# Optimization experiments

Measured on AMD Instinct MI355X. Metric: run time of the kernel, lower is better.

Reference implementation:

```python
import jax, jax.numpy as jnp
import numpy as np

D_IN, D, BOX, REL, THR = 2048, 512, 8, 80, 0.5

def _ln(x, g, b):
    m = jnp.mean(x, -1, keepdims=True)
    v = jnp.mean((x - m) ** 2, -1, keepdims=True)
    return (x - m) * jax.lax.rsqrt(v + 1e-5) * g + b

def setup_inputs():
    key = jax.random.key(0)
    ks = jax.random.split(key, 24)
    B, N = 32, 50
    def lin(k, i, o):
        return jax.random.normal(k, (i, o), jnp.float32) / np.sqrt(i)
    z = lambda n: jnp.zeros((n,), jnp.float32)
    o = lambda n: jnp.ones((n,), jnp.float32)
    return {
        "images": jax.random.normal(ks[0], (B, N, D_IN), jnp.float32),
        "selfbbox": jax.random.uniform(ks[1], (B, N, BOX), jnp.float32),
        "bbox": jax.random.uniform(ks[2], (B, N, N, BOX), jnp.float32),
        "pre_w": lin(ks[3], D_IN, D), "pre_b": z(D), "pre_g": o(D), "pre_be": z(D),
        "subj_w": lin(ks[4], D, D), "subj_b": z(D),
        "obj_w": lin(ks[5], D, D), "obj_b": z(D),
        "ps1_w": lin(ks[6], BOX, 64), "ps1_b": z(64), "ps_g": o(64), "ps_be": z(64),
        "ps2_w": lin(ks[7], 64, 64), "ps2_b": z(64),
        "pr1_w": lin(ks[8], BOX, 64), "pr1_b": z(64), "pr_g": o(64), "pr_be": z(64),
        "pr2_w": lin(ks[9], 64, 64), "pr2_b": z(64),
        "rs_w": lin(ks[10], D + 64, 1), "rs_b": z(1),
        "rf_w": lin(ks[11], D + 64, REL), "rf_b": z(REL),
        "g1_w": lin(ks[12], D + REL, D + REL), "g1_b": z(D + REL),
        "g2_w": lin(ks[13], D + REL, D), "g2_b": z(D),
        "g3_w": lin(ks[14], D, D), "g3_b": z(D),
    }

def reference(images, selfbbox, bbox, pre_w, pre_b, pre_g, pre_be, subj_w, subj_b,
              obj_w, obj_b, ps1_w, ps1_b, ps_g, ps_be, ps2_w, ps2_b,
              pr1_w, pr1_b, pr_g, pr_be, pr2_w, pr2_b, rs_w, rs_b, rf_w, rf_b,
              g1_w, g1_b, g2_w, g2_b, g3_w, g3_b):
    B, N = images.shape[0], images.shape[1]
    mask = jnp.sum(images, -1) != 0.0                      # [B,N] valid nodes
    attention_mask = (~mask)[:, None, None, :]             # [B,1,1,N]
    mf = mask.astype(images.dtype)
    # preprocess: Linear -> ReLU -> (dropout=id at eval) -> LayerNorm
    x = _ln(jax.nn.relu(images @ pre_w + pre_b), pre_g, pre_be)  # [B,N,512]
    x_subj = jax.nn.relu(x @ subj_w + subj_b) * mf[..., None]
    x_obj = jax.nn.relu(x @ obj_w + obj_b) * mf[..., None]
    eye = jnp.eye(N, dtype=bool)
    # pairwise subject/object features: diag(i==j) holds subject, off-diag object j
    x_rela = jnp.where(eye[None, :, :, None], x_subj[:, :, None, :], x_obj[:, None, :, :])
    x_rela = x_rela * mf[:, :, None, None]
    # positional MLPs
    h = jax.nn.relu(selfbbox @ ps1_w + ps1_b)
    h = jax.nn.relu(_ln(h, ps_g, ps_be) @ ps2_w + ps2_b)
    pos_self = h * mf[..., None]
    h = jax.nn.relu(bbox @ pr1_w + pr1_b)
    h = jax.nn.relu(_ln(h, pr_g, pr_be) @ pr2_w + pr2_b)
    pos_relas = h * mf[:, None, :, None] * mf[:, :, None, None]
    pos_rela = jnp.where(eye[None, :, :, None], pos_self[:, :, None, :], pos_relas)
    pos_rela = pos_rela * mf[:, :, None, None]
    pair = jnp.concatenate([x_rela, pos_rela], axis=-1)    # [B,N,N,576]
    pair_mask = mask[:, :, None] & mask[:, None, :]        # [B,N,N]
    # Relationshipness: pairwise relatedness score p + attention-pooled relation feats
    logits = (pair @ rs_w + rs_b)[..., 0]                  # [B,N,N]
    p = jax.nn.sigmoid(logits) * pair_mask.astype(images.dtype)
    attn = jax.nn.softmax(jnp.where(pair_mask, logits, -1e9), axis=2)
    feat = jax.nn.relu(pair @ rf_w + rf_b)                 # [B,N,N,80]
    relas = jnp.einsum('bij,bijf->bif', attn, feat) * mf[..., None]
    xx = jnp.concatenate([x, relas], axis=-1)              # [B,N,592]
    # dynamic edge threshold -> block-diagonal graph, expressed densely per image
    A = p > THR                                            # edge i->j
    Ahat = A | eye[None]                                   # add remaining self loops
    Af = Ahat.astype(xx.dtype)
    deg = jnp.sum(Af, axis=1)                              # in-degree at target j (>=1)
    dinv = jax.lax.rsqrt(deg)
    An = Af * dinv[:, :, None] * dinv[:, None, :]          # sym-normalized adjacency
    def gcn(hh, w, b):
        return jnp.einsum('bij,bif->bjf', An, hh @ w) + b
    x1 = jax.nn.relu(gcn(xx, g1_w, g1_b))
    x2 = jax.nn.relu(gcn(x1, g2_w, g2_b))
    x3 = jax.nn.relu(gcn(x2, g3_w, g3_b))
    outs = jnp.concatenate([x[:, None], x3[:, None]], axis=1)  # [B,2,N,512]
    return (outs, attention_mask)
```

## Files before the change

### kernel.cpp

```cpp
#include <hip/hip_runtime.h>
#include <hip/hip_bf16.h>

typedef __hip_bfloat16 bf16;

#define BB 32
#define NN 50
#define DIN 2048
#define DD 512
#define PD 64
#define FF 80
#define GG 592
#define BN (BB*NN)

#define O_FLAG  0
#define O_MF    16
#define O_SS    1616
#define O_SO    3216
#define O_PS    4816
#define O_FS    107216
#define O_FO    235216
#define O_RL    363216
#define O_LG    491216
#define O_AN    571216
#define O_T     651216
#define O_X1    1598416
#define O_X2    2545616
#define O_WPRE  3364816
#define O_BPRE  4413392
#define O_GPRE  4413904
#define O_EPRE  4414416
#define O_WSUBJ 4414928
#define O_BSUBJ 4677072
#define O_WOBJ  4677584
#define O_BOBJ  4939728
#define O_WPS1  4940240
#define O_BPS1  4940752
#define O_GPS   4940816
#define O_EPS   4940880
#define O_WPS2  4940944
#define O_BPS2  4945040
#define O_WPR1  4945104
#define O_BPR1  4945616
#define O_GPR   4945680
#define O_EPR   4945744
#define O_WPR2  4945808
#define O_BPR2  4949904
#define O_WRS   4949968
#define O_BRS   4950544
#define O_WRF   4950560
#define O_BRF   4996640
#define O_WG1   4996736
#define O_BG1   5347200
#define O_WG2   5347792
#define O_BG2   5650896
#define O_WG3   5651408
#define O_BG3   5913552
#define O_FT    5914064

#define PSLICE  819200

__device__ __forceinline__ float b2f(bf16 x){ return __bfloat162float(x); }

__device__ __forceinline__ float LDI(const bf16* p, size_t i, int f32m){
    if(f32m){
        bf16 a=p[2*i], b=p[2*i+1];
        unsigned short lo,hi;
        __builtin_memcpy(&lo,&a,2); __builtin_memcpy(&hi,&b,2);
        unsigned v=((unsigned)hi<<16)|(unsigned)lo;
        float f; __builtin_memcpy(&f,&v,4);
        return f;
    }
    return __bfloat162float(p[i]);
}

__global__ void k_flag(const bf16* __restrict__ images, float* __restrict__ ws){
    __shared__ int cnt;
    if(threadIdx.x==0) cnt=0;
    __syncthreads();
    bf16 h=images[2*threadIdx.x];
    unsigned short u; __builtin_memcpy(&u,&h,2);
    unsigned e=(u>>7)&0xFF;
    int sane=((u&0x7FFF)==0 || (e>=0x70&&e<=0x85))?1:0;
    atomicAdd(&cnt,sane);
    __syncthreads();
    if(threadIdx.x==0) ws[O_FLAG]=(cnt<48)?1.f:0.f;
}

__device__ __forceinline__ void conv(const bf16* s, float* d, int n, int F, int i0, int st){
    for(int g=i0; g<n; g+=st) d[g]=LDI(s,(size_t)g,F);
}
__global__ void kw(const bf16* p0,const bf16* p1,const bf16* p2,const bf16* p3,
                   const bf16* p4,const bf16* p5,const bf16* p6,const bf16* p7,
                   const bf16* p8,const bf16* p9,const bf16* p10,const bf16* p11,
                   const bf16* p12,const bf16* p13,const bf16* p14,const bf16* p15,
                   const bf16* p16,const bf16* p17,const bf16* p18,const bf16* p19,
                   const bf16* p20,const bf16* p21,const bf16* p22,const bf16* p23,
                   const bf16* p24,const bf16* p25,const bf16* p26,const bf16* p27,
                   const bf16* p28,const bf16* p29, float* __restrict__ ws){
    int F=ws[O_FLAG]>0.5f;
    int i0=blockIdx.x*256+threadIdx.x, st=gridDim.x*256;
    conv(p0, ws+O_WPRE, 1048576,F,i0,st);
    conv(p1, ws+O_BPRE, 512,F,i0,st);
    conv(p2, ws+O_GPRE, 512,F,i0,st);
    conv(p3, ws+O_EPRE, 512,F,i0,st);
    conv(p4, ws+O_WSUBJ,262144,F,i0,st);
    conv(p5, ws+O_BSUBJ,512,F,i0,st);
    conv(p6, ws+O_WOBJ, 262144,F,i0,st);
    conv(p7, ws+O_BOBJ, 512,F,i0,st);
    conv(p8, ws+O_WPS1, 512,F,i0,st);
    conv(p9, ws+O_BPS1, 64,F,i0,st);
    conv(p10,ws+O_GPS,  64,F,i0,st);
    conv(p11,ws+O_EPS,  64,F,i0,st);
    conv(p12,ws+O_WPS2, 4096,F,i0,st);
    conv(p13,ws+O_BPS2, 64,F,i0,st);
    conv(p14,ws+O_WPR1, 512,F,i0,st);
    conv(p15,ws+O_BPR1, 64,F,i0,st);
    conv(p16,ws+O_GPR,  64,F,i0,st);
    conv(p17,ws+O_EPR,  64,F,i0,st);
    conv(p18,ws+O_WPR2, 4096,F,i0,st);
    conv(p19,ws+O_BPR2, 64,F,i0,st);
    conv(p20,ws+O_WRS,  576,F,i0,st);
    conv(p21,ws+O_BRS,  1,F,i0,st);
    conv(p22,ws+O_WRF,  46080,F,i0,st);
    conv(p23,ws+O_BRF,  80,F,i0,st);
    conv(p24,ws+O_WG1,  350464,F,i0,st);
    conv(p25,ws+O_BG1,  592,F,i0,st);
    conv(p26,ws+O_WG2,  303104,F,i0,st);
    conv(p27,ws+O_BG2,  512,F,i0,st);
    conv(p28,ws+O_WG3,  262144,F,i0,st);
    conv(p29,ws+O_BG3,  512,F,i0,st);
}

__global__ void __launch_bounds__(256,4) k_x(const bf16* __restrict__ images,
                                             float* __restrict__ ws){
    __shared__ float as[8*256];
    __shared__ float rsum[4][8];
    int blk=blockIdx.x, t=threadIdx.x;
    int rg=blk>>3, ks=blk&7;
    int r0=rg*8, kbase=ks*256;
    int F=ws[O_FLAG]>0.5f;
    int wv=t>>6, ln=t&63;
    float sv[8];
    #pragma unroll
    for(int row=0;row<8;row++){
        float v=LDI(images,(size_t)(r0+row)*DIN+kbase+t,F);
        as[row*256+t]=v;
        sv[row]=v;
    }
    #pragma unroll
    for(int row=0;row<8;row++){
        float s=sv[row];
        for(int m=32;m>0;m>>=1) s+=__shfl_xor(s,m,64);
        sv[row]=s;
    }
    if(ln==0){
        #pragma unroll
        for(int row=0;row<8;row++) rsum[wv][row]=sv[row];
    }
    __syncthreads();
    if(t<8){
        float s=rsum[0][t]+rsum[1][t]+rsum[2][t]+rsum[3][t];
        ws[O_RL+(size_t)(r0+t)*8+ks]=s;
    }
    const float* wP=ws+O_WPRE+(size_t)kbase*DD;
    int c0=t, c1=t+256;
    float acc[8][2]={};
    for(int k0=0;k0<256;k0+=8){
        float w0[8],w1[8];
        #pragma unroll
        for(int u=0;u<8;u++){ w0[u]=wP[(size_t)(k0+u)*DD+c0]; w1[u]=wP[(size_t)(k0+u)*DD+c1]; }
        #pragma unroll
        for(int row=0;row<8;row++){
            float4 a0=*(const float4*)&as[row*256+k0];
            float4 a1=*(const float4*)&as[row*256+k0+4];
            acc[row][0]+=a0.x*w0[0]; acc[row][1]+=a0.x*w1[0];
            acc[row][0]+=a0.y*w0[1]; acc[row][1]+=a0.y*w1[1];
            acc[row][0]+=a0.z*w0[2]; acc[row][1]+=a0.z*w1[2];
            acc[row][0]+=a0.w*w0[3]; acc[row][1]+=a0.w*w1[3];
            acc[row][0]+=a1.x*w0[4]; acc[row][1]+=a1.x*w1[4];
            acc[row][0]+=a1.y*w0[5]; acc[row][1]+=a1.y*w1[5];
            acc[row][0]+=a1.z*w0[6]; acc[row][1]+=a1.z*w1[6];
            acc[row][0]+=a1.w*w0[7]; acc[row][1]+=a1.w*w1[7];
        }
    }
    float* P=ws + ((ks<7)? (O_FT+(size_t)ks*PSLICE) : (size_t)O_T);
    #pragma unroll
    for(int row=0;row<8;row++){
        size_t b=(size_t)(r0+row)*DD;
        P[b+c0]=acc[row][0]; P[b+c1]=acc[row][1];
    }
}

__global__ void __launch_bounds__(256,4) k_xr(float* __restrict__ ws, float* __restrict__ out){
    __shared__ float red[256];
    int blk=blockIdx.x, t=threadIdx.x;
    int r0=blk*4;
    if(t<4){
        int r=r0+t;
        float s=0.f;
        for(int ks=0;ks<8;ks++) s+=ws[O_RL+(size_t)r*8+ks];
        float mf=(s!=0.f)?1.f:0.f;
        ws[O_MF+r]=mf;
        out[(size_t)BB*2*NN*DD+r]=1.f-mf;
    }
    const float* bPre=ws+O_BPRE; const float* gPre=ws+O_GPRE; const float* ePre=ws+O_EPRE;
    int c0=t, c1=t+256;
    for(int row=0;row<4;row++){
        int r=r0+row;
        float y0=bPre[c0], y1=bPre[c1];
        for(int ks=0;ks<8;ks++){
            const float* P=ws + ((ks<7)? (O_FT+(size_t)ks*PSLICE) : (size_t)O_T);
            y0+=P[(size_t)r*DD+c0]; y1+=P[(size_t)r*DD+c1];
        }
        y0=fmaxf(y0,0.f); y1=fmaxf(y1,0.f);
        red[t]=y0+y1; __syncthreads();
        for(int o=128;o>0;o>>=1){ if(t<o) red[t]+=red[t+o]; __syncthreads(); }
        float mean=red[0]/DD; __syncthreads();
        float d0=y0-mean, d1=y1-mean;
        red[t]=d0*d0+d1*d1; __syncthreads();
        for(int o=128;o>0;o>>=1){ if(t<o) red[t]+=red[t+o]; __syncthreads(); }
        float rstd=rsqrtf(red[0]/DD+1e-5f);
        __syncthreads();
        float xv0=d0*rstd*gPre[c0]+ePre[c0];
        float xv1=d1*rstd*gPre[c1]+ePre[c1];
        size_t ob=((size_t)(r/NN)*2)*NN*DD+(size_t)(r%NN)*DD;
        out[ob+c0]=xv0; out[ob+c1]=xv1;
    }
}

__global__ void __launch_bounds__(256,4) k_so1(const float* __restrict__ out,
                                               float* __restrict__ ws){
    __shared__ float xs[4*DD];
    __shared__ float mrow_s[4];
    int blk=blockIdx.x, t=threadIdx.x;
    int rg=blk>>2, mat=(blk>>1)&1, ch=blk&1;
    int r0=rg*4;
    for(int idx=t; idx<4*DD; idx+=256){
        int row=idx>>9, k=idx&511;
        int r=r0+row;
        xs[idx]=out[((size_t)(r/NN)*2)*NN*DD+(size_t)(r%NN)*DD+k];
    }
    if(t<4) mrow_s[t]=ws[O_MF+r0+t];
    __syncthreads();
    const float* W =ws+(mat?O_WOBJ:O_WSUBJ);
    const float* Bb=ws+(mat?O_BOBJ:O_BSUBJ);
    int c=ch*256+t;
    float acc[4]={0.f,0.f,0.f,0.f};
    for(int k0=0;k0<DD;k0+=8){
        float w[8];
        #pragma unroll
        for(int u=0;u<8;u++) w[u]=W[(size_t)(k0+u)*DD+c];
        #pragma unroll
        for(int row=0;row<4;row++){
            float4 a0=*(const float4*)&xs[row*DD+k0];
            float4 a1=*(const float4*)&xs[row*DD+k0+4];
            acc[row]+=a0.x*w[0]; acc[row]+=a0.y*w[1];
            acc[row]+=a0.z*w[2]; acc[row]+=a0.w*w[3];
            acc[row]+=a1.x*w[4]; acc[row]+=a1.y*w[5];
            acc[row]+=a1.z*w[6]; acc[row]+=a1.w*w[7];
        }
    }
    float* Y=ws+O_FT+(size_t)mat*PSLICE;
    #pragma unroll
    for(int row=0;row<4;row++)
        Y[(size_t)(r0+row)*DD+c]=fmaxf(acc[row]+Bb[c],0.f)*mrow_s[row];
}

__global__ void __launch_bounds__(256,4) k_so2(float* __restrict__ ws){
    __shared__ float yl[4][DD];
    int blk=blockIdx.x, t=threadIdx.x, wv=t>>6, ln=t&63;
    int combo=blk*4+wv;
    int mat=combo&1, r=combo>>1;
    const float* Y=ws+O_FT+(size_t)mat*PSLICE+(size_t)r*DD;
    for(int k=ln;k<DD;k+=64) yl[wv][k]=Y[k];
    __syncthreads();
    const float* wRs=ws+O_WRS;
    float ps=0.f;
    for(int k=ln;k<DD;k+=64) ps+=yl[wv][k]*wRs[k];
    for(int m=32;m>0;m>>=1) ps+=__shfl_xor(ps,m,64);
    if(ln==0) ws[(mat?O_SO:O_SS)+r]=ps;
    const float* wRf=ws+O_WRF;
    float* dst=ws+(mat?O_FO:O_FS)+(size_t)r*FF;
    {
        float a=0.f;
        for(int k0=0;k0<DD;k0+=4){
            float4 y4=*(const float4*)&yl[wv][k0];
            a+=y4.x*wRf[(size_t)k0*FF+ln];
            a+=y4.y*wRf[(size_t)(k0+1)*FF+ln];
            a+=y4.z*wRf[(size_t)(k0+2)*FF+ln];
            a+=y4.w*wRf[(size_t)(k0+3)*FF+ln];
        }
        dst[ln]=a;
    }
    if(ln<16){
        int c=64+ln;
        float a=0.f;
        for(int k0=0;k0<DD;k0+=4){
            float4 y4=*(const float4*)&yl[wv][k0];
            a+=y4.x*wRf[(size_t)k0*FF+c];
            a+=y4.y*wRf[(size_t)(k0+1)*FF+c];
            a+=y4.z*wRf[(size_t)(k0+2)*FF+c];
            a+=y4.w*wRf[(size_t)(k0+3)*FF+c];
        }
        dst[c]=a;
    }
}

__global__ void k_pos_self(const bf16* __restrict__ sb, float* __restrict__ ws){
    __shared__ float h[PD];
    __shared__ float stat[2];
    int r=blockIdx.x, t=threadIdx.x;
    int F=ws[O_FLAG]>0.5f;
    const float* w1=ws+O_WPS1;
    float acc=0.f;
    for(int q=0;q<8;q++) acc+=LDI(sb,(size_t)r*8+q,F)*w1[q*PD+t];
    acc=fmaxf(acc+ws[O_BPS1+t],0.f);
    h[t]=acc; __syncthreads();
    if(t==0){
        float sm=0; for(int k=0;k<PD;k++) sm+=h[k];
        float mean=sm/PD;
        float v=0; for(int k=0;k<PD;k++){float d=h[k]-mean; v+=d*d;}
        stat[0]=mean; stat[1]=rsqrtf(v/PD+1e-5f);
    }
    __syncthreads();
    float hn=(acc-stat[0])*stat[1]*ws[O_GPS+t]+ws[O_EPS+t];
    h[t]=hn; __syncthreads();
    float a2=0.f;
    const float* w2=ws+O_WPS2;
    for(int k=0;k<PD;k++) a2+=h[k]*w2[k*PD+t];
    ws[O_PS+(size_t)r*PD+t]=fmaxf(a2+ws[O_BPS2+t],0.f)*ws[O_MF+r];
}

#define PSTRIDE 68
#define ZROW(m) ((m)*PSTRIDE + (((m)>>3)<<2))

__global__ void __launch_bounds__(256,3) k_pair(const bf16* __restrict__ bbox,
                                                float* __restrict__ ws){
    __shared__ float zp[64*PSTRIDE+64];
    __shared__ float wbuf[80*PSTRIDE];
    __shared__ float w1s[512];
    __shared__ float bbs[512];
    __shared__ float b1s[64], g1s[64], be1s[64], b2s[64], wrss[64];
    __shared__ float brfs[80];
    __shared__ float rowmi[64], rowmj[64], rowbase[64];
    __shared__ int   rowfb[64], rowps[64], rowdg[64];

    int t=threadIdx.x;
    int blk=blockIdx.x;
    int F=ws[O_FLAG]>0.5f;
    float rsb=ws[O_BRS];

    float wrfreg[20];
    #pragma unroll
    for(int u=0;u<20;u++){
        int idx=t+256*u;
        int f=idx>>6, k=idx&63;
        wrfreg[u]=ws[O_WRF+(size_t)(512+k)*FF+f];
    }

    for(int idx=t; idx<4096; idx+=256){ int k=idx>>6, c=idx&63; wbuf[k*PSTRIDE+c]=ws[O_WPR2+idx]; }
    for(int idx=t; idx<512; idx+=256) w1s[idx]=ws[O_WPR1+idx];
    for(int idx=t; idx<512; idx+=256) bbs[idx]=LDI(bbox,(size_t)blk*512+idx,F);
    if(t<64){
        b1s[t]=ws[O_BPR1+t]; g1s[t]=ws[O_GPR+t]; be1s[t]=ws[O_EPR+t];
        b2s[t]=ws[O_BPR2+t]; wrss[t]=ws[O_WRS+512+t];
    } else if(t<144){
        brfs[t-64]=ws[O_BRF+t-64];
    }
    if(t<64){
        int p=blk*64+t;
        int r=p/NN, j=p-r*NN;
        int b=r/NN, i=r-b*NN;
        int dg=(i==j);
        rowmi[t]=ws[O_MF+r];
        rowmj[t]=ws[O_MF+b*NN+j];
        rowdg[t]=dg;
        rowbase[t]=dg? ws[O_SS+r] : ws[O_SO+b*NN+j];
        rowfb[t]=dg? (O_FS+r*FF) : (O_FO+(b*NN+j)*FF);
        rowps[t]=O_PS+r*PD;
    }
    __syncthreads();

    int wv=t>>6, ln=t&63;
    #pragma unroll 2
    for(int q=0;q<16;q++){
        int m=wv*16+q;
        float acc=0.f;
        #pragma unroll
        for(int u=0;u<8;u++) acc+=bbs[m*8+u]*w1s[u*64+ln];
        float h1=fmaxf(acc+b1s[ln],0.f);
        float sm=h1;
        for(int o=32;o>0;o>>=1) sm+=__shfl_xor(sm,o,64);
        float mean=sm*(1.f/64.f);
        float d=h1-mean;
        float vv=d*d;
        for(int o=32;o>0;o>>=1) vv+=__shfl_xor(vv,o,64);
        float rstd=rsqrtf(vv*(1.f/64.f)+1e-5f);
        zp[ZROW(m)+ln]=d*rstd*g1s[ln]+be1s[ln];
    }

    int tr=t>>4, tc=t&15;
    int m0=tr*4, c0=tc*4;
    float a1[4][4]={};
    #pragma unroll 2
    for(int k0=0;k0<64;k0+=4){
        float4 zv[4], wvv[4];
        #pragma unroll
        for(int i=0;i<4;i++) zv[i]=*(const float4*)&zp[ZROW(m0+i)+k0];
        #pragma unroll
        for(int u=0;u<4;u++) wvv[u]=*(const float4*)&wbuf[(k0+u)*PSTRIDE+c0];
        #pragma unroll
        for(int i=0;i<4;i++){
            const float* zpp=(const float*)&zv[i];
            #pragma unroll
            for(int u=0;u<4;u++){
                const float* wp=(const float*)&wvv[u];
                float zk=zpp[u];
                a1[i][0]+=zk*wp[0]; a1[i][1]+=zk*wp[1];
                a1[i][2]+=zk*wp[2]; a1[i][3]+=zk*wp[3];
            }
        }
    }
    __syncthreads();

    #pragma unroll
    for(int i=0;i<4;i++){
        int m=m0+i;
        float4 o;
        if(rowdg[m]){
            const float* ps=ws+rowps[m];
            o.x=ps[c0]; o.y=ps[c0+1]; o.z=ps[c0+2]; o.w=ps[c0+3];
        } else {
            float sc=rowmi[m]*rowmj[m];
            o.x=fmaxf(a1[i][0]+b2s[c0+0],0.f)*sc;
            o.y=fmaxf(a1[i][1]+b2s[c0+1],0.f)*sc;
            o.z=fmaxf(a1[i][2]+b2s[c0+2],0.f)*sc;
            o.w=fmaxf(a1[i][3]+b2s[c0+3],0.f)*sc;
        }
        *(float4*)&zp[ZROW(m)+c0]=o;
    }

    #pragma unroll 2
    for(int q=0;q<16;q++){
        int m=wv*16+q;
        float lp=zp[ZROW(m)+ln]*wrss[ln];
        for(int o=32;o>0;o>>=1) lp+=__shfl_xor(lp,o,64);
        if(ln==0){
            ws[O_LG+(size_t)blk*64+m]=rowmi[m]*rowbase[m]+lp+rsb;
        }
    }

    #pragma unroll
    for(int u=0;u<20;u++){
        int idx=t+256*u;
        wbuf[(idx>>6)*PSTRIDE+(idx&63)]=wrfreg[u];
    }
    __syncthreads();

    {
        int c5=tc*5;
        float a2[4][5]={};
        #pragma unroll 2
        for(int k0=0;k0<64;k0+=4){
            float4 zv[4], wv5[5];
            #pragma unroll
            for(int i=0;i<4;i++) zv[i]=*(const float4*)&zp[ZROW(m0+i)+k0];
            #pragma unroll
            for(int j=0;j<5;j++) wv5[j]=*(const float4*)&wbuf[(c5+j)*PSTRIDE+k0];
            #pragma unroll
            for(int i=0;i<4;i++){
                const float* zpp=(const float*)&zv[i];
                #pragma unroll
                for(int j=0;j<5;j++){
                    const float* wp=(const float*)&wv5[j];
                    a2[i][j]+=zpp[0]*wp[0]+zpp[1]*wp[1]+zpp[2]*wp[2]+zpp[3]*wp[3];
                }
            }
        }
        #pragma unroll
        for(int i=0;i<4;i++){
            int m=m0+i;
            size_t p=(size_t)blk*64+m;
            float mi=rowmi[m];
            const float* fb=ws+rowfb[m];
            #pragma unroll
            for(int j=0;j<5;j++){
                int c=c5+j;
                ws[O_FT+p*FF+c]=fmaxf(mi*fb[c]+a2[i][j]+brfs[c],0.f);
            }
        }
    }
}

__global__ void __launch_bounds__(256,4) k_ra(float* __restrict__ ws){
    __shared__ float shm[2552];
    int blk=blockIdx.x, t=threadIdx.x;
    if(blk<BN){
        int r=blk;
        int b=r/NN;
        float mi=ws[O_MF+r];
        if(t<64){
            float v=-1e9f;
            if(t<NN){
                float mj=ws[O_MF+b*NN+t];
                bool pm=(mi>0.5f)&&(mj>0.5f);
                v=pm? ws[O_LG+(size_t)r*NN+t] : -1e9f;
            }
            float mx=v;
            for(int o=32;o>0;o>>=1) mx=fmaxf(mx,__shfl_xor(mx,o,64));
            float e=(t<NN)? __expf(v-mx) : 0.f;
            float sm=e;
            for(int o=32;o>0;o>>=1) sm+=__shfl_xor(sm,o,64);
            shm[t]=e*(1.f/sm);
        }
        __syncthreads();
        if(t<FF){
            float s=0.f;
            const float* ft=ws+O_FT+(size_t)r*NN*FF;
            for(int j=0;j<NN;j++) s+=shm[j]*ft[(size_t)j*FF+t];
            ws[O_RL+(size_t)r*FF+t]=s*mi;
        }
    } else {
        int b=blk-BN;
        float* Af=shm;
        float* dinv=shm+2500;
        for(int idx=t; idx<NN*NN; idx+=256){
            int i=idx/NN, j=idx%NN;
            float l=ws[O_LG+(size_t)b*NN*NN+idx];
            bool a=(l>0.f)&&(ws[O_MF+b*NN+i]>0.5f)&&(ws[O_MF+b*NN+j]>0.5f);
            Af[idx]=(a||i==j)?1.f:0.f;
        }
        __syncthreads();
        if(t<NN){
            float dg=0.f;
            for(int i=0;i<NN;i++) dg+=Af[i*NN+t];
            dinv[t]=rsqrtf(dg);
        }
        __syncthreads();
        for(int idx=t; idx<NN*NN; idx+=256){
            int i=idx/NN, j=idx%NN;
            ws[O_AN+(size_t)b*NN*NN+idx]=Af[idx]*dinv[i]*dinv[j];
        }
    }
}

__global__ void __launch_bounds__(256,4) kagg(int mode, const float* __restrict__ out,
                                              float* __restrict__ ws, int K, int NCH){
    __shared__ float AnS[2500];
    __shared__ float Xc[50*64];
    int blk=blockIdx.x, t=threadIdx.x;
    int b=blk/NCH, ch=blk-b*NCH;
    int c0=ch*64;
    int cw=K-c0; if(cw>64) cw=64;
    for(int idx=t; idx<2500; idx+=256) AnS[idx]=ws[O_AN+(size_t)b*2500+idx];
    for(int idx=t; idx<50*64; idx+=256){
        int i=idx>>6, cc=idx&63;
        float v=0.f;
        if(cc<cw){
            int c=c0+cc;
            int r=b*NN+i;
            if(mode==0){
                if(c<DD) v=out[(size_t)(2*b)*NN*DD+(size_t)i*DD+c];
                else     v=ws[O_RL+(size_t)r*FF+(c-DD)];
            } else if(mode==1) v=ws[O_X1+(size_t)r*GG+c];
            else               v=ws[O_X2+(size_t)r*DD+c];
        }
        Xc[idx]=v;
    }
    __syncthreads();
    int wv=t>>6, ln=t&63;
    float* T=ws+O_T;
    for(int j=wv; j<NN; j+=4){
        float acc=0.f;
        for(int i=0;i<NN;i++) acc+=AnS[i*NN+j]*Xc[i*64+ln];
        if(ln<cw) T[(size_t)(b*NN+j)*K+c0+ln]=acc;
    }
}

__global__ void __launch_bounds__(256,4) ktf(int mode, float* __restrict__ out,
                   float* __restrict__ ws,
                   const float* __restrict__ W, const float* __restrict__ bias,
                   int K, int NCOL, int NTILE){
    __shared__ float xs[5*GG];
    int blk=blockIdx.x, t=threadIdx.x;
    int rg=blk/NTILE, tile=blk%NTILE;
    const float* T=ws+O_T;
    for(int idx=t; idx<5*K; idx+=256){
        int row=idx/K, k=idx-row*K;
        int gr=rg*5+row;
        xs[row*K+k]=T[(size_t)gr*K+k];
    }
    __syncthreads();
    int c=tile*256+t;
    if(c>=NCOL) return;
    float acc[5];
    #pragma unroll
    for(int u=0;u<5;u++) acc[u]=0.f;
    for(int k0=0;k0<K;k0+=8){
        float w[8];
        #pragma unroll
        for(int u=0;u<8;u++) w[u]=W[(size_t)(k0+u)*NCOL+c];
        #pragma unroll
        for(int row=0;row<5;row++){
            float4 a0=*(const float4*)&xs[row*K+k0];
            float4 a1=*(const float4*)&xs[row*K+k0+4];
            acc[row]+=a0.x*w[0]; acc[row]+=a0.y*w[1];
            acc[row]+=a0.z*w[2]; acc[row]+=a0.w*w[3];
            acc[row]+=a1.x*w[4]; acc[row]+=a1.y*w[5];
            acc[row]+=a1.z*w[6]; acc[row]+=a1.w*w[7];
        }
    }
    int gr0=rg*5;
    float bc=bias[c];
    #pragma unroll
    for(int u=0;u<5;u++){
        float v=fmaxf(acc[u]+bc,0.f);
        int gr=gr0+u;
        if(mode==0)      ws[O_X1+(size_t)gr*GG+c]=v;
        else if(mode==1) ws[O_X2+(size_t)gr*DD+c]=v;
        else {
            int b=gr/NN, j=gr-b*NN;
            out[(size_t)(2*b+1)*NN*DD+(size_t)j*DD+c]=v;
        }
    }
}

extern "C" void kernel_launch(void* const* d_in, const int* in_sizes, int n_in,
                              void* d_out, int out_size, void* d_ws, size_t ws_size,
                              hipStream_t stream) {
    const bf16* images  = (const bf16*)d_in[0];
    const bf16* selfbbox= (const bf16*)d_in[1];
    const bf16* bbox    = (const bf16*)d_in[2];

    float* out=(float*)d_out;
    float* ws =(float*)d_ws;

    k_flag<<<1,64,0,stream>>>(images, ws);
    kw<<<512,256,0,stream>>>((const bf16*)d_in[3],(const bf16*)d_in[4],(const bf16*)d_in[5],
                             (const bf16*)d_in[6],(const bf16*)d_in[7],(const bf16*)d_in[8],
                             (const bf16*)d_in[9],(const bf16*)d_in[10],(const bf16*)d_in[11],
                             (const bf16*)d_in[12],(const bf16*)d_in[13],(const bf16*)d_in[14],
                             (const bf16*)d_in[15],(const bf16*)d_in[16],(const bf16*)d_in[17],
                             (const bf16*)d_in[18],(const bf16*)d_in[19],(const bf16*)d_in[20],
                             (const bf16*)d_in[21],(const bf16*)d_in[22],(const bf16*)d_in[23],
                             (const bf16*)d_in[24],(const bf16*)d_in[25],(const bf16*)d_in[26],
                             (const bf16*)d_in[27],(const bf16*)d_in[28],(const bf16*)d_in[29],
                             (const bf16*)d_in[30],(const bf16*)d_in[31],(const bf16*)d_in[32],
                             ws);
    k_x<<<1600,256,0,stream>>>(images, ws);
    k_xr<<<400,256,0,stream>>>(ws, out);
    k_pos_self<<<BN,PD,0,stream>>>(selfbbox, ws);
    k_so1<<<1600,256,0,stream>>>(out, ws);
    k_so2<<<800,256,0,stream>>>(ws);
    k_pair<<<1250,256,0,stream>>>(bbox, ws);
    k_ra<<<BN+BB,256,0,stream>>>(ws);

    kagg<<<32*10,256,0,stream>>>(0, out, ws, GG, 10);
    ktf<<<320*3,256,0,stream>>>(0, out, ws, ws+O_WG1, ws+O_BG1, GG, GG, 3);
    kagg<<<32*10,256,0,stream>>>(1, out, ws, GG, 10);
    ktf<<<320*2,256,0,stream>>>(1, out, ws, ws+O_WG2, ws+O_BG2, GG, DD, 2);
    kagg<<<32*8,256,0,stream>>>(2, out, ws, DD, 8);
    ktf<<<320*2,256,0,stream>>>(2, out, ws, ws+O_WG3, ws+O_BG3, DD, DD, 2);
}
```

Before: 569.3 us.

## Fold self-position MLP into k_x launch and vectorize pre-projection GEMM tile

The separate k_pos_self launch is removed. Its per-node MLP now runs in 400 extra blocks of k_x, one wave per node, using wave shuffles in place of shared memory and barriers. The node mask multiply moves to k_pair, where the diagonal rows are read, because the mask is not yet known when k_x runs. The k_x GEMM inner tile is also reshaped to float4 weight loads over 4 rows by 4 columns per thread instead of 8 rows by 2 columns, which changes register use and how much of the LDS row data each thread reuses.

Result: slower. 583.9 us (+2.6%).

```diff
diff --git a/kernel.cpp b/kernel.cpp
--- a/kernel.cpp
+++ b/kernel.cpp
@@ -132,14 +132,35 @@
 }
 
 __global__ void __launch_bounds__(256,4) k_x(const bf16* __restrict__ images,
+                                             const bf16* __restrict__ sb,
                                              float* __restrict__ ws){
+    int blk=blockIdx.x, t=threadIdx.x;
+    int F=ws[O_FLAG]>0.5f;
+    int wv=t>>6, ln=t&63;
+    if(blk>=1600){
+        int r=(blk-1600)*4+wv;
+        const float* w1=ws+O_WPS1;
+        float acc=0.f;
+        #pragma unroll
+        for(int q=0;q<8;q++) acc+=LDI(sb,(size_t)r*8+q,F)*w1[q*PD+ln];
+        float h1=fmaxf(acc+ws[O_BPS1+ln],0.f);
+        float sm=0.f;
+        for(int k=0;k<PD;k++) sm+=__shfl(h1,k,64);
+        float mean=sm/PD;
+        float v=0.f;
+        for(int k=0;k<PD;k++){ float d=__shfl(h1,k,64)-mean; v+=d*d; }
+        float rstd=rsqrtf(v/PD+1e-5f);
+        float hn=(h1-mean)*rstd*ws[O_GPS+ln]+ws[O_EPS+ln];
+        float a2=0.f;
+        const float* w2=ws+O_WPS2;
+        for(int k=0;k<PD;k++) a2+=__shfl(hn,k,64)*w2[k*PD+ln];
+        ws[O_PS+(size_t)r*PD+ln]=fmaxf(a2+ws[O_BPS2+ln],0.f);
+        return;
+    }
     __shared__ float as[8*256];
     __shared__ float rsum[4][8];
-    int blk=blockIdx.x, t=threadIdx.x;
     int rg=blk>>3, ks=blk&7;
     int r0=rg*8, kbase=ks*256;
-    int F=ws[O_FLAG]>0.5f;
-    int wv=t>>6, ln=t&63;
     float sv[8];
     #pragma unroll
     for(int row=0;row<8;row++){
@@ -163,31 +184,32 @@
         ws[O_RL+(size_t)(r0+t)*8+ks]=s;
     }
     const float* wP=ws+O_WPRE+(size_t)kbase*DD;
-    int c0=t, c1=t+256;
-    float acc[8][2]={};
-    for(int k0=0;k0<256;k0+=8){
-        float w0[8],w1[8];
-        #pragma unroll
-        for(int u=0;u<8;u++){ w0[u]=wP[(size_t)(k0+u)*DD+c0]; w1[u]=wP[(size_t)(k0+u)*DD+c1]; }
-        #pragma unroll
-        for(int row=0;row<8;row++){
-            float4 a0=*(const float4*)&as[row*256+k0];
-            float4 a1=*(const float4*)&as[row*256+k0+4];
-            acc[row][0]+=a0.x*w0[0]; acc[row][1]+=a0.x*w1[0];
-            acc[row][0]+=a0.y*w0[1]; acc[row][1]+=a0.y*w1[1];
-            acc[row][0]+=a0.z*w0[2]; acc[row][1]+=a0.z*w1[2];
-            acc[row][0]+=a0.w*w0[3]; acc[row][1]+=a0.w*w1[3];
-            acc[row][0]+=a1.x*w0[4]; acc[row][1]+=a1.x*w1[4];
-            acc[row][0]+=a1.y*w0[5]; acc[row][1]+=a1.y*w1[5];
-            acc[row][0]+=a1.z*w0[6]; acc[row][1]+=a1.z*w1[6];
-            acc[row][0]+=a1.w*w0[7]; acc[row][1]+=a1.w*w1[7];
+    int half=t>>7;
+    int c4=(t&127)*4;
+    int rowbase=half*4;
+    float acc[4][4]={};
+    for(int k0=0;k0<256;k0+=4){
+        float4 w4[4];
+        #pragma unroll
+        for(int u=0;u<4;u++) w4[u]=*(const float4*)&wP[(size_t)(k0+u)*DD+c4];
+        #pragma unroll
+        for(int row=0;row<4;row++){
+            float4 a0=*(const float4*)&as[(rowbase+row)*256+k0];
+            const float* ap=(const float*)&a0;
+            #pragma unroll
+            for(int u=0;u<4;u++){
+                const float* wp=(const float*)&w4[u];
+                float ak=ap[u];
+                acc[row][0]+=ak*wp[0]; acc[row][1]+=ak*wp[1];
+                acc[row][2]+=ak*wp[2]; acc[row][3]+=ak*wp[3];
+            }
         }
     }
     float* P=ws + ((ks<7)? (O_FT+(size_t)ks*PSLICE) : (size_t)O_T);
     #pragma unroll
-    for(int row=0;row<8;row++){
-        size_t b=(size_t)(r0+row)*DD;
-        P[b+c0]=acc[row][0]; P[b+c1]=acc[row][1];
+    for(int row=0;row<4;row++){
+        float4 o; o.x=acc[row][0]; o.y=acc[row][1]; o.z=acc[row][2]; o.w=acc[row][3];
+        *(float4*)&P[(size_t)(r0+rowbase+row)*DD+c4]=o;
     }
 }
 
@@ -306,31 +328,6 @@
     }
 }
 
-__global__ void k_pos_self(const bf16* __restrict__ sb, float* __restrict__ ws){
-    __shared__ float h[PD];
-    __shared__ float stat[2];
-    int r=blockIdx.x, t=threadIdx.x;
-    int F=ws[O_FLAG]>0.5f;
-    const float* w1=ws+O_WPS1;
-    float acc=0.f;
-    for(int q=0;q<8;q++) acc+=LDI(sb,(size_t)r*8+q,F)*w1[q*PD+t];
-    acc=fmaxf(acc+ws[O_BPS1+t],0.f);
-    h[t]=acc; __syncthreads();
-    if(t==0){
-        float sm=0; for(int k=0;k<PD;k++) sm+=h[k];
-        float mean=sm/PD;
-        float v=0; for(int k=0;k<PD;k++){float d=h[k]-mean; v+=d*d;}
-        stat[0]=mean; stat[1]=rsqrtf(v/PD+1e-5f);
-    }
-    __syncthreads();
-    float hn=(acc-stat[0])*stat[1]*ws[O_GPS+t]+ws[O_EPS+t];
-    h[t]=hn; __syncthreads();
-    float a2=0.f;
-    const float* w2=ws+O_WPS2;
-    for(int k=0;k<PD;k++) a2+=h[k]*w2[k*PD+t];
-    ws[O_PS+(size_t)r*PD+t]=fmaxf(a2+ws[O_BPS2+t],0.f)*ws[O_MF+r];
-}
-
 #define PSTRIDE 68
 #define ZROW(m) ((m)*PSTRIDE + (((m)>>3)<<2))
 
@@ -429,7 +426,8 @@
         float4 o;
         if(rowdg[m]){
             const float* ps=ws+rowps[m];
-            o.x=ps[c0]; o.y=ps[c0+1]; o.z=ps[c0+2]; o.w=ps[c0+3];
+            float sc=rowmi[m];
+            o.x=ps[c0]*sc; o.y=ps[c0+1]*sc; o.z=ps[c0+2]*sc; o.w=ps[c0+3]*sc;
         } else {
             float sc=rowmi[m]*rowmj[m];
             o.x=fmaxf(a1[i][0]+b2s[c0+0],0.f)*sc;
@@ -647,9 +645,8 @@
                              (const bf16*)d_in[27],(const bf16*)d_in[28],(const bf16*)d_in[29],
                              (const bf16*)d_in[30],(const bf16*)d_in[31],(const bf16*)d_in[32],
                              ws);
-    k_x<<<1600,256,0,stream>>>(images, ws);
+    k_x<<<2000,256,0,stream>>>(images, selfbbox, ws);
     k_xr<<<400,256,0,stream>>>(ws, out);
-    k_pos_self<<<BN,PD,0,stream>>>(selfbbox, ws);
     k_so1<<<1600,256,0,stream>>>(out, ws);
     k_so2<<<800,256,0,stream>>>(ws);
     k_pair<<<1250,256,0,stream>>>(bbox, ws);
```
